# Performance work log

Measured on AMD Instinct MI355X. Metric: run time of the kernel, lower is better.

The kernel has to match this reference:

```python
import jax, jax.numpy as jnp
import numpy as np

EMBED = 256

def _resize(x, h, w):
    # bilinear, half-pixel centers == torch align_corners=False
    B, C = x.shape[:2]
    return jax.image.resize(x, (B, C, h, w), method='bilinear')

def _conv(x, w, b, pad):
    y = jax.lax.conv_general_dilated(x, w, (1, 1), [(pad, pad), (pad, pad)],
                                     dimension_numbers=('NCHW', 'OIHW', 'NCHW'))
    return y + b[None, :, None, None]

def _box1d(x, r, axis):
    # windowed sum over [i-r, i+r], window clipped at borders
    x = jnp.moveaxis(x, axis, -1)
    n = x.shape[-1]
    c = jnp.cumsum(x, axis=-1)
    idx = jnp.arange(n)
    hi = c[..., jnp.clip(idx + r, 0, n - 1)]
    lo_i = idx - r - 1
    lo = jnp.where(lo_i >= 0, c[..., jnp.clip(lo_i, 0, n - 1)], 0.0)
    return jnp.moveaxis(hi - lo, -1, axis)

def _box_mean(x, r):
    # mean filter over (2r+1)^2 window, normalized by valid pixel count at borders
    H, W = x.shape[-2:]
    s = _box1d(_box1d(x, r, -2), r, -1)
    ch = _box1d(jnp.ones((H,), x.dtype), r, 0)
    cw = _box1d(jnp.ones((W,), x.dtype), r, 0)
    return s / (ch[:, None] * cw[None, :])

def _guided_filter(I, p, r, eps):
    # He et al. guided filter. I: (H,W) guide, p: (C,H,W) src, vectorized over C
    mean_I = _box_mean(I, r)
    var_I = _box_mean(I * I, r) - mean_I ** 2
    mean_p = _box_mean(p, r)
    cov_Ip = _box_mean(I[None] * p, r) - mean_I[None] * mean_p
    a = cov_Ip / (var_I[None] + eps)
    b = mean_p - a * mean_I[None]
    return _box_mean(a, r) * I[None] + _box_mean(b, r)

def _forward(fg, bg, mask, feat, w1, b1, w2, b2, w3, b3, wm, bm):
    h2, w2d = 2 * mask.shape[2], 2 * mask.shape[3]
    mask_2x_raw = _resize(mask, h2, w2d)
    feat_2x_raw = _resize(feat, h2, w2d)
    fg_2x = _resize(fg, h2, w2d)
    bg_2x = _resize(bg, h2, w2d)
    x = jnp.concatenate((mask_2x_raw, fg_2x, bg_2x, feat_2x_raw), axis=1)
    x = jax.nn.relu(_conv(x, w1, b1, 0))
    feat_2x = jax.nn.relu(_conv(x, w2, b2, 2))
    guide = jnp.mean(fg_2x, axis=1)[0] * 128.0  # (H2, W2)
    r = int(0.01 * h2)  # static shape -> python int, jit-safe
    filt = _guided_filter(guide, feat_2x[0], r, 0.01)[None]  # (1,C,H2,W2)
    feat_2x = jax.nn.relu(_conv(filt, w3, b3, 0))
    mask_2x = jax.nn.sigmoid(_conv(feat_2x, wm, bm, 0))
    return mask_2x, feat_2x

def setup_inputs():
    key = jax.random.key(0)
    ks = jax.random.split(key, 8)
    E = EMBED
    return {
        'fg': jax.random.normal(ks[0], (1, 3, 128, 128), jnp.float32),
        'bg': jax.random.normal(ks[1], (1, 3, 128, 128), jnp.float32),
        'mask': jax.random.uniform(ks[2], (1, 1, 128, 128), dtype=jnp.float32),
        'feat': jax.random.normal(ks[3], (1, E, 128, 128), jnp.float32),
        'w1': jax.random.normal(ks[4], (E, E + 7, 1, 1), jnp.float32) * 0.05,
        'b1': jnp.zeros((E,), jnp.float32),
        'w2': jax.random.normal(ks[5], (E, E, 5, 5), jnp.float32) * 0.02,
        'b2': jnp.zeros((E,), jnp.float32),
        'w3': jax.random.normal(ks[6], (E, E, 1, 1), jnp.float32) * 0.05,
        'b3': jnp.zeros((E,), jnp.float32),
        'wm': jax.random.normal(ks[7], (1, E, 1, 1), jnp.float32) * 0.05,
        'bm': jnp.zeros((1,), jnp.float32),
    }

def reference(fg, bg, mask, feat, w1, b1, w2, b2, w3, b3, wm, bm):
    return _forward(fg, bg, mask, feat, w1, b1, w2, b2, w3, b3, wm, bm)
```

## Files before the change

kernel.cpp:

```cpp
#include <hip/hip_runtime.h>
#include <hip/hip_bf16.h>
#include <hip/hip_fp16.h>
#include <math.h>


#define P2 65536
#define PADW 260

typedef short  frag8  __attribute__((ext_vector_type(8)));
typedef float  f32x4  __attribute__((ext_vector_type(4)));

__device__ __forceinline__ void load16_lds(const void* gsrc, void* lds) {
    __builtin_amdgcn_global_load_lds((const __attribute__((address_space(1))) void*)gsrc,
                                     (__attribute__((address_space(3))) void*)lds, 16, 0, 0);
}

struct BilC { int y0, y1, x0, x1; float wy0, wy1, wx0, wx1; };
__device__ __forceinline__ BilC bil_coords(int oy, int ox) {
    BilC c;
    int m = oy >> 1;
    if ((oy & 1) == 0) { c.y0 = (m > 0) ? m - 1 : 0; c.y1 = m; c.wy0 = 0.25f; }
    else               { c.y0 = m; c.y1 = (m < 127) ? m + 1 : 127; c.wy0 = 0.75f; }
    c.wy1 = 1.0f - c.wy0;
    int n = ox >> 1;
    if ((ox & 1) == 0) { c.x0 = (n > 0) ? n - 1 : 0; c.x1 = n; c.wx0 = 0.25f; }
    else               { c.x0 = n; c.x1 = (n < 127) ? n + 1 : 127; c.wx0 = 0.75f; }
    c.wx1 = 1.0f - c.wx0;
    return c;
}
__device__ __forceinline__ float bil_eval(const float* __restrict__ src, const BilC& c) {
    return c.wy0 * (c.wx0 * src[c.y0 * 128 + c.x0] + c.wx1 * src[c.y0 * 128 + c.x1])
         + c.wy1 * (c.wx0 * src[c.y1 * 128 + c.x0] + c.wx1 * src[c.y1 * 128 + c.x1]);
}

__global__ __launch_bounds__(256) void prep_mega(const float* __restrict__ mask,
                                                 const float* __restrict__ fg,
                                                 const float* __restrict__ bg,
                                                 const float* __restrict__ feat,
                                                 const float* __restrict__ w1,
                                                 const float* __restrict__ w2,
                                                 const float* __restrict__ w3,
                                                 __hip_bfloat16* __restrict__ xp,
                                                 float* __restrict__ guide,
                                                 float* __restrict__ meanI,
                                                 float* __restrict__ varI,
                                                 __hip_bfloat16* __restrict__ wpk1,
                                                 __hip_bfloat16* __restrict__ wpk2,
                                                 __hip_bfloat16* __restrict__ wpk3,
                                                 __hip_bfloat16* __restrict__ y1p,
                                                 float* __restrict__ haccum) {
    __shared__ float G[20 * 21];
    int b = blockIdx.x;
    int tid = threadIdx.x;
    if (b < 9216) {
        int chunk = b >> 8;
        int p = (b & 255) * 256 + tid;
        union { __hip_bfloat16 h[8]; f32x4 v; } u;
        if (chunk >= 33) {
            f32x4 z = {0.f, 0.f, 0.f, 0.f};
            *(f32x4*)&xp[((size_t)chunk * P2 + p) * 8] = z;
            return;
        }
        BilC bc = bil_coords(p >> 8, p & 255);
#pragma unroll
        for (int j = 0; j < 8; j++) {
            int c = chunk * 8 + j;
            float v = 0.f;
            if (c < 263) {
                const float* src = (c == 0) ? mask
                                 : (c < 4)  ? fg + (c - 1) * 16384
                                 : (c < 7)  ? bg + (c - 4) * 16384
                                 :            feat + (c - 7) * 16384;
                v = bil_eval(src, bc);
            }
            u.h[j] = __float2bfloat16(v);
        }
        *(f32x4*)&xp[((size_t)chunk * P2 + p) * 8] = u.v;
    } else if (b < 9472) {
        int bb = b - 9216;
        int gx0 = (bb & 15) * 16, gy0 = (bb >> 4) * 16;
        for (int i = tid; i < 400; i += 256) {
            int r = i / 20, c = i - r * 20;
            int gy = gy0 + r - 2, gx = gx0 + c - 2;
            float v = 0.f;
            if ((unsigned)gy < 256u && (unsigned)gx < 256u) {
                BilC bc = bil_coords(gy, gx);
                v = (bil_eval(fg, bc) + bil_eval(fg + 16384, bc) + bil_eval(fg + 32768, bc))
                    * (128.0f / 3.0f);
            }
            G[r * 21 + c] = v;
        }
        __syncthreads();
        int ty = tid >> 4, tx = tid & 15;
        int gy = gy0 + ty, gx = gx0 + tx;
        float s = 0.f, ss = 0.f;
#pragma unroll
        for (int dy = 0; dy < 5; dy++)
#pragma unroll
            for (int dx = 0; dx < 5; dx++) {
                float v = G[(ty + dy) * 21 + tx + dx];
                s += v; ss += v * v;
            }
        int cy = ((gy + 2 < 255) ? gy + 2 : 255) - ((gy - 2 > 0) ? gy - 2 : 0) + 1;
        int cx = ((gx + 2 < 255) ? gx + 2 : 255) - ((gx - 2 > 0) ? gx - 2 : 0) + 1;
        float inv = 1.0f / (float)(cy * cx);
        float m = s * inv;
        guide[gy * 256 + gx] = G[(ty + 2) * 21 + tx + 2];
        meanI[gy * 256 + gx] = m;
        varI[gy * 256 + gx]  = ss * inv - m * m;
    } else if (b < 9601) {
        int idx = (b - 9472) * 256 + tid;
        if (idx >= 33024) return;
        int pid = idx >> 4, chunk = idx & 15;
        int py, px;
        if (pid < 520)       { py = pid / 260;               px = pid - py * 260; }
        else if (pid < 1040) { int t = pid - 520; int r = t / 260; py = 258 + r; px = t - r * 260; }
        else                 { int t = pid - 1040; int r = t >> 2; int c = t & 3;
                               py = 2 + r; px = (c < 2) ? c : 256 + c; }
        f32x4 z = {0.f, 0.f, 0.f, 0.f};
        f32x4* dst = (f32x4*)&y1p[((size_t)py * PADW + px) * 256 + chunk * 16];
        dst[0] = z; dst[1] = z;
    } else if (b < 9665) {
        int idx = (b - 9601) * 256 + tid;
        f32x4 z = {0.f, 0.f, 0.f, 0.f};
        *(f32x4*)&haccum[idx * 4] = z;
    } else if (b < 10465) {
        int idx = (b - 9665) * 256 + tid;
        int lane = idx & 63;
        int nb = (idx >> 6) & 15;
        int kt = (idx >> 10) & 7;
        int t  = idx >> 13;
        int oc = nb * 16 + (lane & 15);
        int ic0 = kt * 32 + (lane >> 4) * 8;
        union { __hip_bfloat16 h[8]; f32x4 v; } u;
#pragma unroll
        for (int j = 0; j < 8; j++)
            u.h[j] = __float2bfloat16(w2[(oc * 256 + ic0 + j) * 25 + t]);
        *(f32x4*)&wpk2[(size_t)idx * 8] = u.v;
    } else {
        const float* W; __hip_bfloat16* dst; int K, KT, idx;
        if (b < 10501) { W = w1; dst = wpk1; K = 263; KT = 9; idx = (b - 10465) * 256 + tid; }
        else           { W = w3; dst = wpk3; K = 256; KT = 8; idx = (b - 10501) * 256 + tid; }
        if (idx >= KT * 16 * 64) return;
        int lane = idx & 63;
        int nbg = (idx >> 6) & 15;
        int kt = idx >> 10;
        int oc = nbg * 16 + (lane & 15);
        int ic0 = kt * 32 + (lane >> 4) * 8;
        union { __hip_bfloat16 h[8]; f32x4 v; } u;
#pragma unroll
        for (int j = 0; j < 8; j++) {
            int ic = ic0 + j;
            u.h[j] = (ic < K) ? __float2bfloat16(W[(size_t)oc * K + ic]) : __float2bfloat16(0.f);
        }
        *(f32x4*)&dst[(size_t)idx * 8] = u.v;
    }
}

template<int MODE>
__global__ __launch_bounds__(256) void mfma_1x1(const __hip_bfloat16* __restrict__ xch,
                                                const __hip_bfloat16* __restrict__ wpk,
                                                const float* __restrict__ bias,
                                                void* __restrict__ outp, int KT,
                                                const float* __restrict__ wmv,
                                                float* __restrict__ haccum) {
    __shared__ __align__(16) char smem[MODE == 0 ? 67584 : 49152];
    __hip_bfloat16* Asm0 = (__hip_bfloat16*)smem;
    __hip_bfloat16* Bsm0 = (__hip_bfloat16*)(smem + 16384);
    const int tid = threadIdx.x;
    const int wave = tid >> 6, lane = tid & 63;
    const int q = lane >> 4, m16 = lane & 15;
    const int wn = wave;
    const int pb = blockIdx.x * 128;

    f32x4 acc[8][4] = {};

    auto stA = [&](int kt, int buf) {
#pragma unroll
        for (int it = 0; it < 2; it++) {
            int chb = it * 256 + wave * 64;
            int ch = chb + lane;
            int px = ch >> 2, oct = ch & 3;
            const __hip_bfloat16* src = xch + ((size_t)(kt * 4 + oct) * P2 + pb + px) * 8;
            load16_lds(src, &Asm0[(size_t)buf * 4096 + chb * 8]);
        }
    };
    auto stB = [&](int kt, int buf) {
#pragma unroll
        for (int it = 0; it < 4; it++) {
            int chb = it * 256 + wave * 64;
            int ch = chb + lane;
            int nb = ch >> 6, l = ch & 63;
            const __hip_bfloat16* src = wpk + (((size_t)kt * 16 + nb) * 64 + l) * 8;
            load16_lds(src, &Bsm0[(size_t)buf * 8192 + chb * 8]);
        }
    };
    stA(0, 0); stB(0, 0);
    int buf = 0;
    for (int kt = 0; kt < KT; kt++) {
        __syncthreads();
        if (kt + 1 < KT) { stA(kt + 1, buf ^ 1); stB(kt + 1, buf ^ 1); }
        frag8 a[8], b[4];
#pragma unroll
        for (int i = 0; i < 8; i++)
            a[i] = *(const frag8*)&Asm0[(size_t)buf * 4096 + (i * 16 + m16) * 32 + q * 8];
#pragma unroll
        for (int j = 0; j < 4; j++)
            b[j] = *(const frag8*)&Bsm0[(size_t)buf * 8192 + ((wn * 4 + j) * 64 + lane) * 8];
#pragma unroll
        for (int i = 0; i < 8; i++)
#pragma unroll
            for (int j = 0; j < 4; j++)
                acc[i][j] = __builtin_amdgcn_mfma_f32_16x16x32_bf16(a[i], b[j], acc[i][j], 0, 0, 0);
        buf ^= 1;
    }
    if (MODE == 0) {
        __syncthreads();
        __hip_bfloat16* Ct = (__hip_bfloat16*)smem;
#pragma unroll
        for (int j = 0; j < 4; j++) {
            int ocr = (wn * 4 + j) * 16 + m16;
            float bj = bias[ocr];
#pragma unroll
            for (int i = 0; i < 8; i++) {
                f32x4 v = acc[i][j];
#pragma unroll
                for (int e = 0; e < 4; e++) {
                    int pxr = i * 16 + q * 4 + e;
                    float tv = v[e] + bj;
                    Ct[pxr * 264 + ocr] = __float2bfloat16(tv > 0.f ? tv : 0.f);
                }
            }
        }
        __syncthreads();
        __hip_bfloat16* y1p = (__hip_bfloat16*)outp;
        int colr = (tid & 31) * 8;
#pragma unroll
        for (int it = 0; it < 16; it++) {
            int pxr = it * 8 + (tid >> 5);
            int pix = pb + pxr;
            int py = pix >> 8, px = pix & 255;
            f32x4 val = *(f32x4*)&Ct[pxr * 264 + colr];
            *(f32x4*)&y1p[((size_t)(py + 2) * PADW + px + 2) * 256 + colr] = val;
        }
    } else {
        float* outf = (float*)outp;
        float hpart[8][4] = {};
#pragma unroll
        for (int j = 0; j < 4; j++) {
            int oc = (wn * 4 + j) * 16 + m16;
            float bj = bias[oc];
            float wj = wmv[oc];
#pragma unroll
            for (int i = 0; i < 8; i++) {
                f32x4 v = acc[i][j];
#pragma unroll
                for (int e = 0; e < 4; e++) {
                    float tv = v[e] + bj;
                    tv = tv > 0.f ? tv : 0.f;
                    v[e] = tv;
                    hpart[i][e] += wj * tv;
                }
                *(f32x4*)&outf[(size_t)oc * P2 + pb + i * 16 + q * 4] = v;
            }
        }
#pragma unroll
        for (int i = 0; i < 8; i++)
#pragma unroll
            for (int e = 0; e < 4; e++) {
                float s = hpart[i][e];
                s += __shfl_xor(s, 1);
                s += __shfl_xor(s, 2);
                s += __shfl_xor(s, 4);
                s += __shfl_xor(s, 8);
                if (m16 == 0)
                    atomicAdd(&haccum[pb + i * 16 + q * 4 + e], s);
            }
    }
}

__global__ __launch_bounds__(128, 2) void conv5x5_mfma(const __hip_bfloat16* __restrict__ y1p,
                                                       const __hip_bfloat16* __restrict__ wpk,
                                                       const float* __restrict__ bias,
                                                       __half* __restrict__ pf) {
    __shared__ __align__(16) __hip_bfloat16 Asm[2][12 * 20 * 32];
    const int tid = threadIdx.x;
    const int wave = tid >> 6;
    const int lane = tid & 63;
    const int q = lane >> 4;
    const int m16 = lane & 15;
    const int bx = blockIdx.x, by = blockIdx.y, oh = blockIdx.z;

    f32x4 acc[4][8] = {};

    auto stageA = [&](int ict, int buf) {
#pragma unroll
        for (int g = 0; g < 8; g++) {
            int grp = g * 2 + wave;
            if (grp >= 15) break;
            int chb = grp * 64;
            int ch = chb + lane;
            int oct = ch & 3, pl = ch >> 2;
            int pc = pl % 20, pr = pl / 20;
            const __hip_bfloat16* src =
                y1p + (size_t)((by * 8 + pr) * PADW + bx * 16 + pc) * 256 + ict * 32 + oct * 8;
            load16_lds(src, &Asm[buf][chb * 8]);
        }
    };
    auto loadB = [&](int s, frag8* dst) {
        int ict = s / 25, tap = s - ict * 25;
        const __hip_bfloat16* base =
            wpk + ((size_t)((tap * 8 + ict) * 16 + oh * 8) * 64 + lane) * 8;
#pragma unroll
        for (int j = 0; j < 8; j++)
            dst[j] = *(const frag8*)(base + (size_t)j * 512);
    };

    frag8 bA[8], bB[8];
    stageA(0, 0);
    loadB(0, bA);
    int abuf = 0;

    auto step = [&](int s, frag8* bcur, frag8* bnxt) {
        int ict = s / 25, tap = s - ict * 25;
        if (tap == 0) __syncthreads();
        if (s + 1 < 200) loadB(s + 1, bnxt);
        if (tap == 24 && ict < 7) stageA(ict + 1, abuf ^ 1);
        int dy = tap / 5, dx = tap - dy * 5;
        frag8 a[4];
#pragma unroll
        for (int i = 0; i < 4; i++)
            a[i] = *(const frag8*)&Asm[abuf][((wave * 4 + i + dy) * 20 + m16 + dx) * 32 + q * 8];
#pragma unroll
        for (int i = 0; i < 4; i++)
#pragma unroll
            for (int j = 0; j < 8; j++)
                acc[i][j] = __builtin_amdgcn_mfma_f32_16x16x32_bf16(a[i], bcur[j], acc[i][j], 0, 0, 0);
        if (tap == 24) abuf ^= 1;
    };
    for (int s = 0; s < 200; s += 2) { step(s, bA, bB); step(s + 1, bB, bA); }

#pragma unroll
    for (int j = 0; j < 8; j++) {
        int oc = oh * 128 + j * 16 + m16;
        float bj = bias[oc];
#pragma unroll
        for (int i = 0; i < 4; i++) {
            int r = wave * 4 + i;
            f32x4 v = acc[i][j];
            union { __half h[4]; double d; } u;
#pragma unroll
            for (int e = 0; e < 4; e++) {
                float t = v[e] + bj;
                u.h[e] = __float2half(t > 0.f ? t : 0.f);
            }
            *(double*)&pf[(size_t)oc * P2 + (by * 8 + r) * 256 + bx * 16 + q * 4] = u.d;
        }
    }
}

__global__ __launch_bounds__(256) void gf_stream(const __half* __restrict__ p,
                                                 const float* __restrict__ guide,
                                                 const float* __restrict__ meanI,
                                                 const float* __restrict__ varI,
                                                 __hip_bfloat16* __restrict__ filt) {
    __shared__ float Prow[260], IProw[260], Arow[260], Brow[260];
    const int t = threadIdx.x;
    const int c = blockIdx.y;
    const int Y0 = blockIdx.x * 64;
    const __half* pc = p + (size_t)c * P2;
    if (t < 4) {
        int e = (t < 2) ? t : 256 + t;
        Prow[e] = 0.f; IProw[e] = 0.f; Arow[e] = 0.f; Brow[e] = 0.f;
    }
    int xlo = (t - 2 > 0) ? t - 2 : 0, xhi = (t + 2 < 255) ? t + 2 : 255;
    const float cxr = 1.0f / (float)(xhi - xlo + 1);
    float hp[5] = {0, 0, 0, 0, 0}, hip[5] = {0, 0, 0, 0, 0};
    float ha[5] = {0, 0, 0, 0, 0}, hb[5] = {0, 0, 0, 0, 0};
    float vp = 0.f, vip = 0.f, va = 0.f, vb = 0.f;
    __syncthreads();
    for (int s = 0; s < 72; s++) {
        int yL = Y0 - 4 + s;
        bool okL = ((unsigned)yL < 256u);
        if (okL) {
            float pv = __half2float(pc[yL * 256 + t]);
            Prow[t + 2] = pv;
            IProw[t + 2] = guide[yL * 256 + t] * pv;
        }
        __syncthreads();
        float hpn = 0.f, hipn = 0.f;
        if (okL) {
            hpn  = Prow[t] + Prow[t + 1] + Prow[t + 2] + Prow[t + 3] + Prow[t + 4];
            hipn = IProw[t] + IProw[t + 1] + IProw[t + 2] + IProw[t + 3] + IProw[t + 4];
        }
        vp += hpn - hp[0];  vip += hipn - hip[0];
        hp[0] = hp[1]; hp[1] = hp[2]; hp[2] = hp[3]; hp[3] = hp[4]; hp[4] = hpn;
        hip[0] = hip[1]; hip[1] = hip[2]; hip[2] = hip[3]; hip[3] = hip[4]; hip[4] = hipn;
        int yA = yL - 2;
        float aV = 0.f, bV = 0.f;
        if ((unsigned)yA < 256u && yA >= Y0 - 2) {
            int ylo = (yA - 2 > 0) ? yA - 2 : 0, yhi = (yA + 2 < 255) ? yA + 2 : 255;
            float inv1 = cxr / (float)(yhi - ylo + 1);
            float mI = meanI[yA * 256 + t], vI = varI[yA * 256 + t];
            float mp = vp * inv1, mip = vip * inv1;
            float cov = mip - mI * mp;
            aV = cov / (vI + 0.01f);
            bV = mp - aV * mI;
        }
        Arow[t + 2] = aV;
        Brow[t + 2] = bV;
        __syncthreads();
        float han = Arow[t] + Arow[t + 1] + Arow[t + 2] + Arow[t + 3] + Arow[t + 4];
        float hbn = Brow[t] + Brow[t + 1] + Brow[t + 2] + Brow[t + 3] + Brow[t + 4];
        va += han - ha[0];  vb += hbn - hb[0];
        ha[0] = ha[1]; ha[1] = ha[2]; ha[2] = ha[3]; ha[3] = ha[4]; ha[4] = han;
        hb[0] = hb[1]; hb[1] = hb[2]; hb[2] = hb[3]; hb[3] = hb[4]; hb[4] = hbn;
        int yo = yL - 4;
        if (yo >= Y0 && yo < Y0 + 64 && (unsigned)yo < 256u) {
            int ylo = (yo - 2 > 0) ? yo - 2 : 0, yhi = (yo + 2 < 255) ? yo + 2 : 255;
            float inv2 = cxr / (float)(yhi - ylo + 1);
            float I = guide[yo * 256 + t];
            filt[(size_t)c * P2 + yo * 256 + t] = __float2bfloat16((va * I + vb) * inv2);
        }
    }
}

__global__ void transpose_cp(const __hip_bfloat16* __restrict__ filt,
                             __hip_bfloat16* __restrict__ filtp) {
    __shared__ __hip_bfloat16 T[8][1032];
    int tid = threadIdx.x;
    int p0 = blockIdx.x * 1024;
    int cg = blockIdx.y;
    for (int i = tid; i < 4096; i += 256) {
        int r = i >> 9, pl2 = (i & 511) * 2;
        unsigned v = *(const unsigned*)&filt[(size_t)(cg * 8 + r) * P2 + p0 + pl2];
        *(unsigned*)&T[r][pl2] = v;
    }
    __syncthreads();
    for (int pl = tid; pl < 1024; pl += 256) {
        union { __hip_bfloat16 h[8]; f32x4 v; } u;
#pragma unroll
        for (int j = 0; j < 8; j++) u.h[j] = T[j][pl];
        *(f32x4*)&filtp[((size_t)cg * P2 + p0 + pl) * 8] = u.v;
    }
}

__global__ void sigmoid_head(const float* __restrict__ haccum, const float* __restrict__ bm,
                             float* __restrict__ out) {
    int p = blockIdx.x * 256 + threadIdx.x;
    out[p] = 1.0f / (1.0f + expf(-(haccum[p] + bm[0])));
}

extern "C" void kernel_launch(void* const* d_in, const int* in_sizes, int n_in,
                              void* d_out, int out_size, void* d_ws, size_t ws_size,
                              hipStream_t stream) {
    const float* fg   = (const float*)d_in[0];
    const float* bg   = (const float*)d_in[1];
    const float* mask = (const float*)d_in[2];
    const float* feat = (const float*)d_in[3];
    const float* w1   = (const float*)d_in[4];
    const float* b1   = (const float*)d_in[5];
    const float* w2   = (const float*)d_in[6];
    const float* b2   = (const float*)d_in[7];
    const float* w3   = (const float*)d_in[8];
    const float* b3   = (const float*)d_in[9];
    const float* wm   = (const float*)d_in[10];
    const float* bm   = (const float*)d_in[11];
    float* out = (float*)d_out;
    char* w8 = (char*)d_ws;

    __half* pbuf          = (__half*)w8;
    __hip_bfloat16* filtp = (__hip_bfloat16*)(w8 + 33554432);
    __hip_bfloat16* xp    = (__hip_bfloat16*)(w8 + 67108864);
    __hip_bfloat16* filt  = (__hip_bfloat16*)(w8 + 67108864);
    __hip_bfloat16* y1p   = (__hip_bfloat16*)(w8 + 104857600);
    __hip_bfloat16* wpk2  = (__hip_bfloat16*)(w8 + 139468800);
    __hip_bfloat16* wpk1  = (__hip_bfloat16*)(w8 + 142745600);
    __hip_bfloat16* wpk3  = (__hip_bfloat16*)(w8 + 142893056);
    float* guide  = (float*)(w8 + 143024128);
    float* meanI  = guide + P2;
    float* varI   = meanI + P2;
    float* haccum = varI + P2;

    prep_mega<<<10533, 256, 0, stream>>>(mask, fg, bg, feat, w1, w2, w3,
                                         xp, guide, meanI, varI, wpk1, wpk2, wpk3, y1p, haccum);
    mfma_1x1<0><<<512, 256, 0, stream>>>(xp, wpk1, b1, y1p, 9, nullptr, nullptr);
    conv5x5_mfma<<<dim3(16, 32, 2), 128, 0, stream>>>(y1p, wpk2, b2, pbuf);
    gf_stream<<<dim3(4, 256), 256, 0, stream>>>(pbuf, guide, meanI, varI, filt);
    transpose_cp<<<dim3(64, 32), 256, 0, stream>>>(filt, filtp);
    mfma_1x1<1><<<512, 256, 0, stream>>>(filtp, wpk3, b3, out + P2, 8, wm, haccum);
    sigmoid_head<<<256, 256, 0, stream>>>(haccum, bm, out);
}
```

Baseline: 431.5 us.

## Apply first 1x1 conv at low resolution before bilinear upsampling

Result: no change. 429.2 us (-0.6%).

```diff
diff --git a/kernel.cpp b/kernel.cpp
--- a/kernel.cpp
+++ b/kernel.cpp
@@ -5,14 +5,21 @@
 
 
 #define P2 65536
+#define PLO 16384
 #define PADW 260
 
 typedef short  frag8  __attribute__((ext_vector_type(8)));
 typedef float  f32x4  __attribute__((ext_vector_type(4)));
+typedef short  s16x8  __attribute__((ext_vector_type(8)));
 
 __device__ __forceinline__ void load16_lds(const void* gsrc, void* lds) {
     __builtin_amdgcn_global_load_lds((const __attribute__((address_space(1))) void*)gsrc,
                                      (__attribute__((address_space(3))) void*)lds, 16, 0, 0);
+}
+__device__ __forceinline__ float bf2f(short s) {
+    union { unsigned u; float f; } c;
+    c.u = ((unsigned)(unsigned short)s) << 16;
+    return c.f;
 }
 
 struct BilC { int y0, y1, x0, x1; float wy0, wy1, wx0, wx1; };
@@ -40,7 +47,7 @@
                                                  const float* __restrict__ w1,
                                                  const float* __restrict__ w2,
                                                  const float* __restrict__ w3,
-                                                 __hip_bfloat16* __restrict__ xp,
+                                                 __hip_bfloat16* __restrict__ xlo,
                                                  float* __restrict__ guide,
                                                  float* __restrict__ meanI,
                                                  float* __restrict__ varI,
@@ -52,32 +59,32 @@
     __shared__ float G[20 * 21];
     int b = blockIdx.x;
     int tid = threadIdx.x;
-    if (b < 9216) {
-        int chunk = b >> 8;
-        int p = (b & 255) * 256 + tid;
+    if (b < 2304) {
+        int idx = b * 256 + tid;
+        int chunk = idx >> 14;
+        int px = idx & 16383;
         union { __hip_bfloat16 h[8]; f32x4 v; } u;
         if (chunk >= 33) {
             f32x4 z = {0.f, 0.f, 0.f, 0.f};
-            *(f32x4*)&xp[((size_t)chunk * P2 + p) * 8] = z;
+            *(f32x4*)&xlo[((size_t)chunk * PLO + px) * 8] = z;
             return;
         }
-        BilC bc = bil_coords(p >> 8, p & 255);
 #pragma unroll
         for (int j = 0; j < 8; j++) {
             int c = chunk * 8 + j;
             float v = 0.f;
             if (c < 263) {
                 const float* src = (c == 0) ? mask
-                                 : (c < 4)  ? fg + (c - 1) * 16384
-                                 : (c < 7)  ? bg + (c - 4) * 16384
-                                 :            feat + (c - 7) * 16384;
-                v = bil_eval(src, bc);
+                                 : (c < 4)  ? fg + (c - 1) * PLO
+                                 : (c < 7)  ? bg + (c - 4) * PLO
+                                 :            feat + (c - 7) * PLO;
+                v = src[px];
             }
             u.h[j] = __float2bfloat16(v);
         }
-        *(f32x4*)&xp[((size_t)chunk * P2 + p) * 8] = u.v;
-    } else if (b < 9472) {
-        int bb = b - 9216;
+        *(f32x4*)&xlo[((size_t)chunk * PLO + px) * 8] = u.v;
+    } else if (b < 2560) {
+        int bb = b - 2304;
         int gx0 = (bb & 15) * 16, gy0 = (bb >> 4) * 16;
         for (int i = tid; i < 400; i += 256) {
             int r = i / 20, c = i - r * 20;
@@ -85,7 +92,7 @@
             float v = 0.f;
             if ((unsigned)gy < 256u && (unsigned)gx < 256u) {
                 BilC bc = bil_coords(gy, gx);
-                v = (bil_eval(fg, bc) + bil_eval(fg + 16384, bc) + bil_eval(fg + 32768, bc))
+                v = (bil_eval(fg, bc) + bil_eval(fg + PLO, bc) + bil_eval(fg + 2 * PLO, bc))
                     * (128.0f / 3.0f);
             }
             G[r * 21 + c] = v;
@@ -108,8 +115,8 @@
         guide[gy * 256 + gx] = G[(ty + 2) * 21 + tx + 2];
         meanI[gy * 256 + gx] = m;
         varI[gy * 256 + gx]  = ss * inv - m * m;
-    } else if (b < 9601) {
-        int idx = (b - 9472) * 256 + tid;
+    } else if (b < 2689) {
+        int idx = (b - 2560) * 256 + tid;
         if (idx >= 33024) return;
         int pid = idx >> 4, chunk = idx & 15;
         int py, px;
@@ -120,12 +127,12 @@
         f32x4 z = {0.f, 0.f, 0.f, 0.f};
         f32x4* dst = (f32x4*)&y1p[((size_t)py * PADW + px) * 256 + chunk * 16];
         dst[0] = z; dst[1] = z;
-    } else if (b < 9665) {
-        int idx = (b - 9601) * 256 + tid;
+    } else if (b < 2753) {
+        int idx = (b - 2689) * 256 + tid;
         f32x4 z = {0.f, 0.f, 0.f, 0.f};
         *(f32x4*)&haccum[idx * 4] = z;
-    } else if (b < 10465) {
-        int idx = (b - 9665) * 256 + tid;
+    } else if (b < 3553) {
+        int idx = (b - 2753) * 256 + tid;
         int lane = idx & 63;
         int nb = (idx >> 6) & 15;
         int kt = (idx >> 10) & 7;
@@ -139,8 +146,8 @@
         *(f32x4*)&wpk2[(size_t)idx * 8] = u.v;
     } else {
         const float* W; __hip_bfloat16* dst; int K, KT, idx;
-        if (b < 10501) { W = w1; dst = wpk1; K = 263; KT = 9; idx = (b - 10465) * 256 + tid; }
-        else           { W = w3; dst = wpk3; K = 256; KT = 8; idx = (b - 10501) * 256 + tid; }
+        if (b < 3589) { W = w1; dst = wpk1; K = 263; KT = 9; idx = (b - 3553) * 256 + tid; }
+        else          { W = w3; dst = wpk3; K = 256; KT = 8; idx = (b - 3589) * 256 + tid; }
         if (idx >= KT * 16 * 64) return;
         int lane = idx & 63;
         int nbg = (idx >> 6) & 15;
@@ -157,6 +164,109 @@
     }
 }
 
+__global__ __launch_bounds__(256) void gemm_z(const __hip_bfloat16* __restrict__ xlo,
+                                              const __hip_bfloat16* __restrict__ wpk,
+                                              const float* __restrict__ bias,
+                                              __hip_bfloat16* __restrict__ z) {
+    __shared__ __align__(16) char smem[34816];
+    __hip_bfloat16* Asm0 = (__hip_bfloat16*)smem;
+    __hip_bfloat16* Bsm0 = (__hip_bfloat16*)(smem + 16384);
+    const int tid = threadIdx.x;
+    const int wave = tid >> 6, lane = tid & 63;
+    const int q = lane >> 4, m16 = lane & 15;
+    const int wm = wave & 1, wn = wave >> 1;
+    const int pb = blockIdx.x * 128, oh = blockIdx.y;
+
+    f32x4 acc[4][4] = {};
+
+    auto stA = [&](int kt, int buf) {
+#pragma unroll
+        for (int it = 0; it < 2; it++) {
+            int chb = it * 256 + wave * 64;
+            int ch = chb + lane;
+            int px = ch >> 2, oct = ch & 3;
+            const __hip_bfloat16* src = xlo + ((size_t)(kt * 4 + oct) * PLO + pb + px) * 8;
+            load16_lds(src, &Asm0[(size_t)buf * 4096 + chb * 8]);
+        }
+    };
+    auto stB = [&](int kt, int buf) {
+#pragma unroll
+        for (int it = 0; it < 2; it++) {
+            int chb = it * 256 + wave * 64;
+            int ch = chb + lane;
+            int nb = ch >> 6, l = ch & 63;
+            const __hip_bfloat16* src = wpk + (((size_t)kt * 16 + oh * 8 + nb) * 64 + l) * 8;
+            load16_lds(src, &Bsm0[(size_t)buf * 4096 + chb * 8]);
+        }
+    };
+    stA(0, 0); stB(0, 0);
+    int buf = 0;
+    for (int kt = 0; kt < 9; kt++) {
+        __syncthreads();
+        if (kt + 1 < 9) { stA(kt + 1, buf ^ 1); stB(kt + 1, buf ^ 1); }
+        frag8 a[4], b[4];
+#pragma unroll
+        for (int i = 0; i < 4; i++)
+            a[i] = *(const frag8*)&Asm0[(size_t)buf * 4096 + ((wm * 4 + i) * 16 + m16) * 32 + q * 8];
+#pragma unroll
+        for (int j = 0; j < 4; j++)
+            b[j] = *(const frag8*)&Bsm0[(size_t)buf * 4096 + ((wn * 4 + j) * 64 + lane) * 8];
+#pragma unroll
+        for (int i = 0; i < 4; i++)
+#pragma unroll
+            for (int j = 0; j < 4; j++)
+                acc[i][j] = __builtin_amdgcn_mfma_f32_16x16x32_bf16(a[i], b[j], acc[i][j], 0, 0, 0);
+        buf ^= 1;
+    }
+    __syncthreads();
+    __hip_bfloat16* Ct = (__hip_bfloat16*)smem;
+#pragma unroll
+    for (int j = 0; j < 4; j++) {
+        int ocr = (wn * 4 + j) * 16 + m16;
+        float bj = bias[oh * 128 + ocr];
+#pragma unroll
+        for (int i = 0; i < 4; i++) {
+            f32x4 v = acc[i][j];
+#pragma unroll
+            for (int e = 0; e < 4; e++) {
+                int pxr = (wm * 4 + i) * 16 + q * 4 + e;
+                Ct[pxr * 136 + ocr] = __float2bfloat16(v[e] + bj);
+            }
+        }
+    }
+    __syncthreads();
+    int colr = (tid & 15) * 8;
+    int cg = oh * 16 + (tid & 15);
+#pragma unroll
+    for (int it = 0; it < 8; it++) {
+        int pxr = it * 16 + (tid >> 4);
+        f32x4 val = *(f32x4*)&Ct[pxr * 136 + colr];
+        *(f32x4*)&z[((size_t)cg * PLO + pb + pxr) * 8] = val;
+    }
+}
+
+__global__ __launch_bounds__(256) void upsample_y1(const __hip_bfloat16* __restrict__ z,
+                                                   __hip_bfloat16* __restrict__ y1p) {
+    int t = blockIdx.x * 256 + threadIdx.x;
+    int cg = t & 31;
+    int p = t >> 5;
+    int py = p >> 8, pxx = p & 255;
+    BilC c = bil_coords(py, pxx);
+    const __hip_bfloat16* zc = z + (size_t)cg * PLO * 8;
+    s16x8 t00 = *(const s16x8*)&zc[(c.y0 * 128 + c.x0) * 8];
+    s16x8 t01 = *(const s16x8*)&zc[(c.y0 * 128 + c.x1) * 8];
+    s16x8 t10 = *(const s16x8*)&zc[(c.y1 * 128 + c.x0) * 8];
+    s16x8 t11 = *(const s16x8*)&zc[(c.y1 * 128 + c.x1) * 8];
+    union { __hip_bfloat16 h[8]; f32x4 v; } o;
+#pragma unroll
+    for (int j = 0; j < 8; j++) {
+        float v = c.wy0 * (c.wx0 * bf2f(t00[j]) + c.wx1 * bf2f(t01[j]))
+                + c.wy1 * (c.wx0 * bf2f(t10[j]) + c.wx1 * bf2f(t11[j]));
+        o.h[j] = __float2bfloat16(v > 0.f ? v : 0.f);
+    }
+    *(f32x4*)&y1p[((size_t)(py + 2) * PADW + pxx + 2) * 256 + cg * 8] = o.v;
+}
+
 template<int MODE>
 __global__ __launch_bounds__(256) void mfma_1x1(const __hip_bfloat16* __restrict__ xch,
                                                 const __hip_bfloat16* __restrict__ wpk,
@@ -164,7 +274,7 @@
                                                 void* __restrict__ outp, int KT,
                                                 const float* __restrict__ wmv,
                                                 float* __restrict__ haccum) {
-    __shared__ __align__(16) char smem[MODE == 0 ? 67584 : 49152];
+    __shared__ __align__(16) char smem[49152];
     __hip_bfloat16* Asm0 = (__hip_bfloat16*)smem;
     __hip_bfloat16* Bsm0 = (__hip_bfloat16*)(smem + 16384);
     const int tid = threadIdx.x;
@@ -214,36 +324,7 @@
                 acc[i][j] = __builtin_amdgcn_mfma_f32_16x16x32_bf16(a[i], b[j], acc[i][j], 0, 0, 0);
         buf ^= 1;
     }
-    if (MODE == 0) {
-        __syncthreads();
-        __hip_bfloat16* Ct = (__hip_bfloat16*)smem;
-#pragma unroll
-        for (int j = 0; j < 4; j++) {
-            int ocr = (wn * 4 + j) * 16 + m16;
-            float bj = bias[ocr];
-#pragma unroll
-            for (int i = 0; i < 8; i++) {
-                f32x4 v = acc[i][j];
-#pragma unroll
-                for (int e = 0; e < 4; e++) {
-                    int pxr = i * 16 + q * 4 + e;
-                    float tv = v[e] + bj;
-                    Ct[pxr * 264 + ocr] = __float2bfloat16(tv > 0.f ? tv : 0.f);
-                }
-            }
-        }
-        __syncthreads();
-        __hip_bfloat16* y1p = (__hip_bfloat16*)outp;
-        int colr = (tid & 31) * 8;
-#pragma unroll
-        for (int it = 0; it < 16; it++) {
-            int pxr = it * 8 + (tid >> 5);
-            int pix = pb + pxr;
-            int py = pix >> 8, px = pix & 255;
-            f32x4 val = *(f32x4*)&Ct[pxr * 264 + colr];
-            *(f32x4*)&y1p[((size_t)(py + 2) * PADW + px + 2) * 256 + colr] = val;
-        }
-    } else {
+    {
         float* outf = (float*)outp;
         float hpart[8][4] = {};
 #pragma unroll
@@ -471,8 +552,9 @@
 
     __half* pbuf          = (__half*)w8;
     __hip_bfloat16* filtp = (__hip_bfloat16*)(w8 + 33554432);
-    __hip_bfloat16* xp    = (__hip_bfloat16*)(w8 + 67108864);
     __hip_bfloat16* filt  = (__hip_bfloat16*)(w8 + 67108864);
+    __hip_bfloat16* xlo   = (__hip_bfloat16*)(w8 + 67108864);
+    __hip_bfloat16* zbuf  = (__hip_bfloat16*)(w8 + 76546048);
     __hip_bfloat16* y1p   = (__hip_bfloat16*)(w8 + 104857600);
     __hip_bfloat16* wpk2  = (__hip_bfloat16*)(w8 + 139468800);
     __hip_bfloat16* wpk1  = (__hip_bfloat16*)(w8 + 142745600);
@@ -482,9 +564,10 @@
     float* varI   = meanI + P2;
     float* haccum = varI + P2;
 
-    prep_mega<<<10533, 256, 0, stream>>>(mask, fg, bg, feat, w1, w2, w3,
-                                         xp, guide, meanI, varI, wpk1, wpk2, wpk3, y1p, haccum);
-    mfma_1x1<0><<<512, 256, 0, stream>>>(xp, wpk1, b1, y1p, 9, nullptr, nullptr);
+    prep_mega<<<3621, 256, 0, stream>>>(mask, fg, bg, feat, w1, w2, w3,
+                                        xlo, guide, meanI, varI, wpk1, wpk2, wpk3, y1p, haccum);
+    gemm_z<<<dim3(128, 2), 256, 0, stream>>>(xlo, wpk1, b1, zbuf);
+    upsample_y1<<<8192, 256, 0, stream>>>(zbuf, y1p);
     conv5x5_mfma<<<dim3(16, 32, 2), 128, 0, stream>>>(y1p, wpk2, b2, pbuf);
     gf_stream<<<dim3(4, 256), 256, 0, stream>>>(pbuf, guide, meanI, varI, filt);
     transpose_cp<<<dim3(64, 32), 256, 0, stream>>>(filt, filtp);
```
